# Kernel optimization log

Hardware: AMD Instinct MI355X
Metric: run time of the kernel (lower is better)

The kernel has to match this reference:

```python
import jax, jax.numpy as jnp
import numpy as np

N, E, IN, ED, H = 50000, 500000, 27, 12, 128
LAYERS = 3


def _bn(h, g, b):
    # BatchNorm1d, training-mode batch statistics, biased variance, eps=1e-5
    mu = h.mean(0)
    var = h.var(0)
    return (h - mu) * jax.lax.rsqrt(var + 1e-5) * g + b


def _layer(x, src, dst, ea, eps, eW, eb, W1, b1, g1, be1, W2, b2, ng, nb):
    # GINEConv: project edge_attr to node dim, message = relu(x_j + e), sum-aggregate
    e = ea @ eW + eb                                   # [E, in_dim]
    m = jax.nn.relu(x[src] + e)                        # [E, in_dim]
    agg = jax.ops.segment_sum(m, dst, num_segments=N)  # [N, in_dim]
    h = (1.0 + eps) * x + agg
    # conv MLP: Linear -> BN -> ReLU -> (Dropout eval=id) -> Linear
    h = jax.nn.relu(_bn(h @ W1 + b1, g1, be1))
    h = h @ W2 + b2
    # outer BatchNorm -> ReLU -> (Dropout eval=id)
    return jax.nn.relu(_bn(h, ng, nb))


def setup_inputs() -> dict:
    key = jax.random.key(0)
    ks = iter(jax.random.split(key, 64))
    d = {}
    d["x"] = jax.random.normal(next(ks), (N, IN), jnp.float32)
    d["edge_index"] = jax.random.randint(next(ks), (2, E), 0, N, jnp.int32)
    d["edge_attr"] = jax.random.normal(next(ks), (E, ED), jnp.float32)
    for i in range(LAYERS):
        ind = IN if i == 0 else H
        d[f"l{i}_eps"] = jnp.zeros((), jnp.float32)
        d[f"l{i}_eW"] = jax.random.normal(next(ks), (ED, ind), jnp.float32) * 0.1
        d[f"l{i}_eb"] = jnp.zeros((ind,), jnp.float32)
        d[f"l{i}_W1"] = jax.random.normal(next(ks), (ind, 2 * H), jnp.float32) * (1.0 / np.sqrt(ind))
        d[f"l{i}_b1"] = jnp.zeros((2 * H,), jnp.float32)
        d[f"l{i}_g1"] = jnp.ones((2 * H,), jnp.float32)
        d[f"l{i}_be1"] = jnp.zeros((2 * H,), jnp.float32)
        d[f"l{i}_W2"] = jax.random.normal(next(ks), (2 * H, H), jnp.float32) * (1.0 / np.sqrt(2 * H))
        d[f"l{i}_b2"] = jnp.zeros((H,), jnp.float32)
        d[f"l{i}_ng"] = jnp.ones((H,), jnp.float32)
        d[f"l{i}_nb"] = jnp.zeros((H,), jnp.float32)
    return d


def reference(x, edge_index, edge_attr,
              l0_eps, l0_eW, l0_eb, l0_W1, l0_b1, l0_g1, l0_be1, l0_W2, l0_b2, l0_ng, l0_nb,
              l1_eps, l1_eW, l1_eb, l1_W1, l1_b1, l1_g1, l1_be1, l1_W2, l1_b2, l1_ng, l1_nb,
              l2_eps, l2_eW, l2_eb, l2_W1, l2_b1, l2_g1, l2_be1, l2_W2, l2_b2, l2_ng, l2_nb):
    src, dst = edge_index[0], edge_index[1]
    P = [
        (l0_eps, l0_eW, l0_eb, l0_W1, l0_b1, l0_g1, l0_be1, l0_W2, l0_b2, l0_ng, l0_nb),
        (l1_eps, l1_eW, l1_eb, l1_W1, l1_b1, l1_g1, l1_be1, l1_W2, l1_b2, l1_ng, l1_nb),
        (l2_eps, l2_eW, l2_eb, l2_W1, l2_b1, l2_g1, l2_be1, l2_W2, l2_b2, l2_ng, l2_nb),
    ]
    h = x
    for i, p in enumerate(P):
        out = _layer(h, src, dst, edge_attr, *p)
        if 0 < i < LAYERS - 1 and out.shape == h.shape:
            h = h + 0.3 * out
        else:
            h = out
    return h
```

## Files before the change

### kernel.cpp

```cpp
#include <hip/hip_runtime.h>
#include <hip/hip_bf16.h>


typedef __attribute__((ext_vector_type(8))) short bf16x8;
typedef __attribute__((ext_vector_type(4))) float f32x4;

static inline int cdiv(int a, int b) { return (a + b - 1) / b; }

__device__ inline ushort f2bf(float f) {
    uint32_t u = __float_as_uint(f);
    return (ushort)((u + 0x7FFFu + ((u >> 16) & 1u)) >> 16);
}
__device__ inline float bf2f(ushort h) { return __uint_as_float(((uint32_t)h) << 16); }

__global__ __launch_bounds__(256) void histogram_dst(const int* __restrict__ dst,
                                                     int* __restrict__ deg, int E) {
    int i = blockIdx.x * blockDim.x + threadIdx.x;
    int stride = gridDim.x * blockDim.x;
    for (; i < E; i += stride) atomicAdd(&deg[dst[i]], 1);
}

__global__ __launch_bounds__(1024) void scan_deg(const int* __restrict__ deg,
                                                 int* __restrict__ rowptr, int N) {
    __shared__ int part[1024];
    int t = threadIdx.x;
    int chunk = (N + 1023) / 1024;
    int b = t * chunk;
    int e = b + chunk;
    if (b > N) b = N;
    if (e > N) e = N;
    int s = 0;
    for (int i = b; i < e; ++i) s += deg[i];
    part[t] = s;
    __syncthreads();
    for (int off = 1; off < 1024; off <<= 1) {
        int v = (t >= off) ? part[t - off] : 0;
        __syncthreads();
        part[t] += v;
        __syncthreads();
    }
    int base = (t == 0) ? 0 : part[t - 1];
    for (int i = b; i < e; ++i) {
        rowptr[i] = base;
        base += deg[i];
    }
    if (t == 1023) rowptr[N] = base;
}

__global__ __launch_bounds__(256) void scatter_edges(const int* __restrict__ dst,
                                                     int* __restrict__ cursor,
                                                     int* __restrict__ eid, int E) {
    int i = blockIdx.x * blockDim.x + threadIdx.x;
    int stride = gridDim.x * blockDim.x;
    for (; i < E; i += stride) {
        int pos = atomicAdd(&cursor[dst[i]], 1);
        eid[pos] = i;
    }
}

template <int IND>
__global__ __launch_bounds__(256) void gather_kernel(
    const int* __restrict__ rowptr, const int* __restrict__ eid, const int* __restrict__ src,
    const float* __restrict__ ea, const float* __restrict__ eW, const float* __restrict__ eb,
    const float* __restrict__ x, const float* __restrict__ epsp, float* __restrict__ agg, int N) {
    __shared__ __align__(16) float sW[12 * IND];
    __shared__ __align__(16) float sb[IND];
    int tid = threadIdx.x;
    for (int i = tid; i < 12 * IND; i += 256) sW[i] = eW[i];
    for (int i = tid; i < IND; i += 256) sb[i] = eb[i];
    __syncthreads();

    float onePlusEps = 1.0f + *epsp;
    int lane = tid & 31;
    int n = blockIdx.x * 8 + (tid >> 5);
    if (n >= N) return;
    int beg = rowptr[n], end = rowptr[n + 1];

    if constexpr (IND == 128) {
        int d0 = lane << 2;
        float4 acc = make_float4(0.f, 0.f, 0.f, 0.f);
        float4 bb = *(const float4*)&sb[d0];
        int i = beg;
        for (; i + 2 <= end; i += 2) {
            int e0 = eid[i], e1 = eid[i + 1];
            int s0 = src[e0], s1 = src[e1];
            float av0 = (lane < 12) ? ea[(size_t)e0 * 12 + lane] : 0.0f;
            float av1 = (lane < 12) ? ea[(size_t)e1 * 12 + lane] : 0.0f;
            float4 x0 = *(const float4*)&x[(size_t)s0 * 128 + d0];
            float4 x1 = *(const float4*)&x[(size_t)s1 * 128 + d0];
            float4 p0 = bb, p1 = bb;
#pragma unroll
            for (int k = 0; k < 12; ++k) {
                float a0 = __shfl(av0, k, 32);
                float a1 = __shfl(av1, k, 32);
                float4 w = *(const float4*)&sW[k * 128 + d0];
                p0.x = fmaf(a0, w.x, p0.x); p0.y = fmaf(a0, w.y, p0.y);
                p0.z = fmaf(a0, w.z, p0.z); p0.w = fmaf(a0, w.w, p0.w);
                p1.x = fmaf(a1, w.x, p1.x); p1.y = fmaf(a1, w.y, p1.y);
                p1.z = fmaf(a1, w.z, p1.z); p1.w = fmaf(a1, w.w, p1.w);
            }
            acc.x += fmaxf(x0.x + p0.x, 0.f) + fmaxf(x1.x + p1.x, 0.f);
            acc.y += fmaxf(x0.y + p0.y, 0.f) + fmaxf(x1.y + p1.y, 0.f);
            acc.z += fmaxf(x0.z + p0.z, 0.f) + fmaxf(x1.z + p1.z, 0.f);
            acc.w += fmaxf(x0.w + p0.w, 0.f) + fmaxf(x1.w + p1.w, 0.f);
        }
        if (i < end) {
            int e = eid[i];
            int s = src[e];
            float av = (lane < 12) ? ea[(size_t)e * 12 + lane] : 0.0f;
            float4 p = bb;
#pragma unroll
            for (int k = 0; k < 12; ++k) {
                float ak = __shfl(av, k, 32);
                float4 w = *(const float4*)&sW[k * 128 + d0];
                p.x = fmaf(ak, w.x, p.x); p.y = fmaf(ak, w.y, p.y);
                p.z = fmaf(ak, w.z, p.z); p.w = fmaf(ak, w.w, p.w);
            }
            float4 xv = *(const float4*)&x[(size_t)s * 128 + d0];
            acc.x += fmaxf(xv.x + p.x, 0.f);
            acc.y += fmaxf(xv.y + p.y, 0.f);
            acc.z += fmaxf(xv.z + p.z, 0.f);
            acc.w += fmaxf(xv.w + p.w, 0.f);
        }
        float4 xn = *(const float4*)&x[(size_t)n * 128 + d0];
        float4 o;
        o.x = fmaf(onePlusEps, xn.x, acc.x);
        o.y = fmaf(onePlusEps, xn.y, acc.y);
        o.z = fmaf(onePlusEps, xn.z, acc.z);
        o.w = fmaf(onePlusEps, xn.w, acc.w);
        *(float4*)&agg[(size_t)n * 128 + d0] = o;
    } else {
        int d = lane;
        float acc = 0.0f;
        float bb = (d < IND) ? sb[d] : 0.0f;
        for (int i = beg; i < end; ++i) {
            int e = eid[i];
            int s = src[e];
            float av = (lane < 12) ? ea[(size_t)e * 12 + lane] : 0.0f;
            float p = bb;
#pragma unroll
            for (int k = 0; k < 12; ++k) {
                float ak = __shfl(av, k, 32);
                if (d < IND) p = fmaf(ak, sW[k * IND + d], p);
            }
            if (d < IND) acc += fmaxf(x[(size_t)s * IND + d] + p, 0.0f);
        }
        if (d < IND) agg[(size_t)n * IND + d] = fmaf(onePlusEps, x[(size_t)n * IND + d], acc);
    }
}

__global__ __launch_bounds__(256) void repack_w(const float* __restrict__ W, int K, int N,
                                                ushort* __restrict__ hi, ushort* __restrict__ lo) {
    int kg = (K + 31) / 32;
    int total = (N / 16) * kg * 64;
    int idx = blockIdx.x * 256 + threadIdx.x;
    if (idx >= total) return;
    int l = idx & 63;
    int g = (idx >> 6) % kg;
    int t = (idx >> 6) / kg;
#pragma unroll
    for (int j = 0; j < 8; ++j) {
        int k = g * 32 + ((l >> 4) << 3) + j;
        int n = (t << 4) + (l & 15);
        float v = (k < K) ? W[(size_t)k * N + n] : 0.0f;
        ushort h = f2bf(v);
        hi[(size_t)idx * 8 + j] = h;
        lo[(size_t)idx * 8 + j] = f2bf(v - bf2f(h));
    }
}

template <bool PRE_BN>
__global__ __launch_bounds__(256) void mfma_gemm(const float* __restrict__ A, int M, int K,
                                                 const ushort* __restrict__ Wph,
                                                 const ushort* __restrict__ Wpl,
                                                 const float* __restrict__ bias,
                                                 const float* __restrict__ scale,
                                                 const float* __restrict__ shift,
                                                 float* __restrict__ C, int ldc,
                                                 float* __restrict__ sums,
                                                 float* __restrict__ sumsq) {
    __shared__ __align__(16) ushort As_hi[128 * 32];
    __shared__ __align__(16) ushort As_lo[128 * 32];
    int tid = threadIdx.x;
    int lane = tid & 63;
    int wv = tid >> 6;
    int wm = wv >> 1, wn = wv & 1;
    int row0 = blockIdx.x * 128;
    int col0 = blockIdx.y * 64;
    int kg = (K + 31) >> 5;

    f32x4 acc[4][2] = {};

    for (int g = 0; g < kg; ++g) {
        int k0 = g << 5;
        for (int c = tid; c < 1024; c += 256) {
            int row = c >> 3;
            int kc = (c & 7) << 2;
            int gm = row0 + row;
            float v[4] = {0.f, 0.f, 0.f, 0.f};
            if (gm < M) {
                const float* ap = &A[(size_t)gm * K + k0 + kc];
                if (k0 + kc + 4 <= K) {
                    float4 t4 = *(const float4*)ap;
                    v[0] = t4.x; v[1] = t4.y; v[2] = t4.z; v[3] = t4.w;
                } else {
#pragma unroll
                    for (int t = 0; t < 4; ++t)
                        if (k0 + kc + t < K) v[t] = ap[t];
                }
                if (PRE_BN) {
#pragma unroll
                    for (int t = 0; t < 4; ++t) {
                        int k = k0 + kc + t;
                        if (k < K) v[t] = fmaxf(fmaf(v[t], scale[k], shift[k]), 0.0f);
                    }
                }
            }
            ushort h[4], l2[4];
#pragma unroll
            for (int t = 0; t < 4; ++t) {
                h[t] = f2bf(v[t]);
                l2[t] = f2bf(v[t] - bf2f(h[t]));
            }
            int e = row * 32 + kc;
            *(ushort4*)&As_hi[e] = make_ushort4(h[0], h[1], h[2], h[3]);
            *(ushort4*)&As_lo[e] = make_ushort4(l2[0], l2[1], l2[2], l2[3]);
        }
        __syncthreads();

        bf16x8 bh[2], bl[2], ah[4], al[4];
#pragma unroll
        for (int nf = 0; nf < 2; ++nf) {
            int tn = (col0 >> 4) + (wn << 1) + nf;
            size_t off = (((size_t)tn * kg + g) * 64 + lane) * 8;
            bh[nf] = *(const bf16x8*)(Wph + off);
            bl[nf] = *(const bf16x8*)(Wpl + off);
        }
#pragma unroll
        for (int mf = 0; mf < 4; ++mf) {
            int e = ((wm << 6) + (mf << 4) + (lane & 15)) * 32 + ((lane >> 4) << 3);
            ah[mf] = *(const bf16x8*)&As_hi[e];
            al[mf] = *(const bf16x8*)&As_lo[e];
        }
#pragma unroll
        for (int mf = 0; mf < 4; ++mf)
#pragma unroll
            for (int nf = 0; nf < 2; ++nf) {
                acc[mf][nf] =
                    __builtin_amdgcn_mfma_f32_16x16x32_bf16(ah[mf], bh[nf], acc[mf][nf], 0, 0, 0);
                acc[mf][nf] =
                    __builtin_amdgcn_mfma_f32_16x16x32_bf16(ah[mf], bl[nf], acc[mf][nf], 0, 0, 0);
                acc[mf][nf] =
                    __builtin_amdgcn_mfma_f32_16x16x32_bf16(al[mf], bh[nf], acc[mf][nf], 0, 0, 0);
            }
        __syncthreads();
    }

#pragma unroll
    for (int nf = 0; nf < 2; ++nf) {
        int col = col0 + (wn << 5) + (nf << 4) + (lane & 15);
        float bv = bias[col];
        float s = 0.f, qs = 0.f;
#pragma unroll
        for (int mf = 0; mf < 4; ++mf) {
            int rbase = row0 + (wm << 6) + (mf << 4) + ((lane >> 4) << 2);
#pragma unroll
            for (int q = 0; q < 4; ++q) {
                int row = rbase + q;
                if (row < M) {
                    float v = acc[mf][nf][q] + bv;
                    C[(size_t)row * ldc + col] = v;
                    s += v;
                    qs = fmaf(v, v, qs);
                }
            }
        }
        s += __shfl_xor(s, 16);
        s += __shfl_xor(s, 32);
        qs += __shfl_xor(qs, 16);
        qs += __shfl_xor(qs, 32);
        if (lane < 16) {
            atomicAdd(&sums[col], s);
            atomicAdd(&sumsq[col], qs);
        }
    }
}

__global__ void finalize_bn(const float* __restrict__ sums, const float* __restrict__ sumsq,
                            const float* __restrict__ g, const float* __restrict__ b,
                            float* __restrict__ scale, float* __restrict__ shift, int C,
                            float invN) {
    int c = blockIdx.x * blockDim.x + threadIdx.x;
    if (c < C) {
        float mu = sums[c] * invN;
        float var = sumsq[c] * invN - mu * mu;
        float inv = rsqrtf(var + 1e-5f);
        float sc = g[c] * inv;
        scale[c] = sc;
        shift[c] = b[c] - mu * sc;
    }
}

template <bool RES>
__global__ __launch_bounds__(256) void bn_apply(const float* __restrict__ h,
                                                const float* __restrict__ scale,
                                                const float* __restrict__ shift,
                                                const float* __restrict__ xprev,
                                                float* __restrict__ out, int total4) {
    int i = blockIdx.x * blockDim.x + threadIdx.x;
    int stride = gridDim.x * blockDim.x;
    for (; i < total4; i += stride) {
        int c0 = (i & 31) << 2;
        float4 v = ((const float4*)h)[i];
        float4 o;
        o.x = fmaxf(fmaf(v.x, scale[c0 + 0], shift[c0 + 0]), 0.0f);
        o.y = fmaxf(fmaf(v.y, scale[c0 + 1], shift[c0 + 1]), 0.0f);
        o.z = fmaxf(fmaf(v.z, scale[c0 + 2], shift[c0 + 2]), 0.0f);
        o.w = fmaxf(fmaf(v.w, scale[c0 + 3], shift[c0 + 3]), 0.0f);
        if (RES) {
            float4 xp = ((const float4*)xprev)[i];
            o.x = fmaf(0.3f, o.x, xp.x);
            o.y = fmaf(0.3f, o.y, xp.y);
            o.z = fmaf(0.3f, o.z, xp.z);
            o.w = fmaf(0.3f, o.w, xp.w);
        }
        ((float4*)out)[i] = o;
    }
}

extern "C" void kernel_launch(void* const* d_in, const int* in_sizes, int n_in, void* d_out,
                              int out_size, void* d_ws, size_t ws_size, hipStream_t stream) {
    const float* x_in = (const float*)d_in[0];
    const int* ei = (const int*)d_in[1];
    const float* ea = (const float*)d_in[2];
    const int IN_DIM = 27;
    const int H = 128;
    int N = in_sizes[0] / IN_DIM;
    int E = in_sizes[1] / 2;
    const int* src = ei;
    const int* dst = ei + E;

    auto L = [&](int layer, int j) -> const float* {
        return (const float*)d_in[3 + 11 * layer + j];
    };

    float* X0 = (float*)d_ws;
    float* AGG = X0 + (size_t)N * H;
    float* H1 = AGG + (size_t)N * H;
    float* STATS = H1 + (size_t)N * 2 * H;
    float* sums1 = STATS;
    float* sq1 = STATS + 256;
    float* sums2 = STATS + 512;
    float* sq2 = STATS + 640;
    float* scale1 = STATS + 768;
    float* shift1 = STATS + 1024;
    float* scale2 = STATS + 1280;
    float* shift2 = STATS + 1408;
    int* rowptr = (int*)(STATS + 1536);
    int* cursor = rowptr + (N + 1);
    int* eid = cursor + N;
    size_t wp_off = ((size_t)(eid + E - (int*)d_ws) * 4 + 15) & ~(size_t)15;
    ushort* Wp1h = (ushort*)((char*)d_ws + wp_off);
    ushort* Wp1l = Wp1h + 32768;
    ushort* Wp2h = Wp1l + 32768;
    ushort* Wp2l = Wp2h + 32768;
    float* X1 = (float*)d_out;

    float invN = 1.0f / (float)N;
    int gridM = cdiv(N, 128);
    int gatherG = cdiv(N, 8);

    hipMemsetAsync(rowptr, 0, (size_t)(N + 1) * sizeof(int), stream);
    histogram_dst<<<1024, 256, 0, stream>>>(dst, rowptr, E);
    scan_deg<<<1, 1024, 0, stream>>>(rowptr, cursor, N);
    hipMemcpyAsync(rowptr, cursor, (size_t)(N + 1) * sizeof(int), hipMemcpyDeviceToDevice, stream);
    scatter_edges<<<1024, 256, 0, stream>>>(dst, cursor, eid, E);

    for (int i = 0; i < 3; ++i) {
        int ind = (i == 0) ? IN_DIM : H;
        const float* xin = (i == 0) ? x_in : ((i == 1) ? X0 : X1);
        float* xout = (i == 2) ? (float*)d_out : ((i == 0) ? X0 : X1);

        hipMemsetAsync(STATS, 0, 768 * sizeof(float), stream);

        int kg1 = cdiv(ind, 32);
        int tot1 = 16 * kg1 * 64;
        repack_w<<<cdiv(tot1, 256), 256, 0, stream>>>(L(i, 3), ind, 256, Wp1h, Wp1l);
        int tot2 = 8 * 8 * 64;
        repack_w<<<cdiv(tot2, 256), 256, 0, stream>>>(L(i, 7), 256, 128, Wp2h, Wp2l);

        if (i == 0)
            gather_kernel<27><<<gatherG, 256, 0, stream>>>(rowptr, eid, src, ea, L(i, 1), L(i, 2),
                                                           xin, L(i, 0), AGG, N);
        else
            gather_kernel<128><<<gatherG, 256, 0, stream>>>(rowptr, eid, src, ea, L(i, 1), L(i, 2),
                                                            xin, L(i, 0), AGG, N);

        mfma_gemm<false><<<dim3(gridM, 4), 256, 0, stream>>>(AGG, N, ind, Wp1h, Wp1l, L(i, 4),
                                                             nullptr, nullptr, H1, 256, sums1, sq1);
        finalize_bn<<<1, 256, 0, stream>>>(sums1, sq1, L(i, 5), L(i, 6), scale1, shift1, 256, invN);

        mfma_gemm<true><<<dim3(gridM, 2), 256, 0, stream>>>(H1, N, 256, Wp2h, Wp2l, L(i, 8),
                                                            scale1, shift1, AGG, 128, sums2, sq2);
        finalize_bn<<<1, 256, 0, stream>>>(sums2, sq2, L(i, 9), L(i, 10), scale2, shift2, 128,
                                           invN);

        int total4 = N * H / 4;
        if (i == 1)
            bn_apply<true><<<2048, 256, 0, stream>>>(AGG, scale2, shift2, X0, xout, total4);
        else
            bn_apply<false><<<2048, 256, 0, stream>>>(AGG, scale2, shift2, nullptr, xout, total4);
    }
}
```

Measured before the change: 967.6 us.

## Widen GEMM tiles to full N per block, unroll gather by 4, vectorize layer-0 gather

The MFMA GEMM now uses 512-thread blocks that each cover the full output width, so every A row tile is loaded and split into bf16 hi/lo only once instead of once per column block. The 128-wide gather processes four edges per iteration to keep more independent loads in flight. The 27-wide layer-0 gather splits each 32-lane group into four 8-lane subgroups that each handle a different edge with float4 vectors, then reduces the subgroups with shuffles. In exchange, GEMM blocks carry more accumulators and registers, and the layer-0 path has more complex boundary handling.

```diff
diff --git a/kernel.cpp b/kernel.cpp
--- a/kernel.cpp
+++ b/kernel.cpp
@@ -58,16 +58,15 @@
     }
 }
 
-template <int IND>
-__global__ __launch_bounds__(256) void gather_kernel(
+__global__ __launch_bounds__(256) void gather128(
     const int* __restrict__ rowptr, const int* __restrict__ eid, const int* __restrict__ src,
     const float* __restrict__ ea, const float* __restrict__ eW, const float* __restrict__ eb,
     const float* __restrict__ x, const float* __restrict__ epsp, float* __restrict__ agg, int N) {
-    __shared__ __align__(16) float sW[12 * IND];
-    __shared__ __align__(16) float sb[IND];
+    __shared__ __align__(16) float sW[12 * 128];
+    __shared__ __align__(16) float sb[128];
     int tid = threadIdx.x;
-    for (int i = tid; i < 12 * IND; i += 256) sW[i] = eW[i];
-    for (int i = tid; i < IND; i += 256) sb[i] = eb[i];
+    for (int i = tid; i < 12 * 128; i += 256) sW[i] = eW[i];
+    if (tid < 128) sb[tid] = eb[tid];
     __syncthreads();
 
     float onePlusEps = 1.0f + *epsp;
@@ -75,77 +74,171 @@
     int n = blockIdx.x * 8 + (tid >> 5);
     if (n >= N) return;
     int beg = rowptr[n], end = rowptr[n + 1];
-
-    if constexpr (IND == 128) {
-        int d0 = lane << 2;
-        float4 acc = make_float4(0.f, 0.f, 0.f, 0.f);
-        float4 bb = *(const float4*)&sb[d0];
-        int i = beg;
-        for (; i + 2 <= end; i += 2) {
-            int e0 = eid[i], e1 = eid[i + 1];
-            int s0 = src[e0], s1 = src[e1];
-            float av0 = (lane < 12) ? ea[(size_t)e0 * 12 + lane] : 0.0f;
-            float av1 = (lane < 12) ? ea[(size_t)e1 * 12 + lane] : 0.0f;
-            float4 x0 = *(const float4*)&x[(size_t)s0 * 128 + d0];
-            float4 x1 = *(const float4*)&x[(size_t)s1 * 128 + d0];
-            float4 p0 = bb, p1 = bb;
-#pragma unroll
-            for (int k = 0; k < 12; ++k) {
-                float a0 = __shfl(av0, k, 32);
-                float a1 = __shfl(av1, k, 32);
-                float4 w = *(const float4*)&sW[k * 128 + d0];
-                p0.x = fmaf(a0, w.x, p0.x); p0.y = fmaf(a0, w.y, p0.y);
-                p0.z = fmaf(a0, w.z, p0.z); p0.w = fmaf(a0, w.w, p0.w);
-                p1.x = fmaf(a1, w.x, p1.x); p1.y = fmaf(a1, w.y, p1.y);
-                p1.z = fmaf(a1, w.z, p1.z); p1.w = fmaf(a1, w.w, p1.w);
+    int d0 = lane << 2;
+    float4 bb = *(const float4*)&sb[d0];
+    float4 acc = make_float4(0.f, 0.f, 0.f, 0.f);
+
+    int i = beg;
+    for (; i + 4 <= end; i += 4) {
+        int e[4], s[4];
+        float av[4];
+        float4 xv[4], p[4];
+#pragma unroll
+        for (int j = 0; j < 4; ++j) e[j] = eid[i + j];
+#pragma unroll
+        for (int j = 0; j < 4; ++j) {
+            s[j] = src[e[j]];
+            av[j] = (lane < 12) ? ea[(size_t)e[j] * 12 + lane] : 0.0f;
+        }
+#pragma unroll
+        for (int j = 0; j < 4; ++j) {
+            xv[j] = *(const float4*)&x[(size_t)s[j] * 128 + d0];
+            p[j] = bb;
+        }
+#pragma unroll
+        for (int k = 0; k < 12; ++k) {
+            float4 w = *(const float4*)&sW[k * 128 + d0];
+#pragma unroll
+            for (int j = 0; j < 4; ++j) {
+                float a = __shfl(av[j], k, 32);
+                p[j].x = fmaf(a, w.x, p[j].x);
+                p[j].y = fmaf(a, w.y, p[j].y);
+                p[j].z = fmaf(a, w.z, p[j].z);
+                p[j].w = fmaf(a, w.w, p[j].w);
             }
-            acc.x += fmaxf(x0.x + p0.x, 0.f) + fmaxf(x1.x + p1.x, 0.f);
-            acc.y += fmaxf(x0.y + p0.y, 0.f) + fmaxf(x1.y + p1.y, 0.f);
-            acc.z += fmaxf(x0.z + p0.z, 0.f) + fmaxf(x1.z + p1.z, 0.f);
-            acc.w += fmaxf(x0.w + p0.w, 0.f) + fmaxf(x1.w + p1.w, 0.f);
-        }
-        if (i < end) {
-            int e = eid[i];
-            int s = src[e];
-            float av = (lane < 12) ? ea[(size_t)e * 12 + lane] : 0.0f;
-            float4 p = bb;
-#pragma unroll
-            for (int k = 0; k < 12; ++k) {
-                float ak = __shfl(av, k, 32);
-                float4 w = *(const float4*)&sW[k * 128 + d0];
-                p.x = fmaf(ak, w.x, p.x); p.y = fmaf(ak, w.y, p.y);
-                p.z = fmaf(ak, w.z, p.z); p.w = fmaf(ak, w.w, p.w);
+        }
+#pragma unroll
+        for (int j = 0; j < 4; ++j) {
+            acc.x += fmaxf(xv[j].x + p[j].x, 0.f);
+            acc.y += fmaxf(xv[j].y + p[j].y, 0.f);
+            acc.z += fmaxf(xv[j].z + p[j].z, 0.f);
+            acc.w += fmaxf(xv[j].w + p[j].w, 0.f);
+        }
+    }
+    for (; i < end; ++i) {
+        int e = eid[i];
+        int s = src[e];
+        float av = (lane < 12) ? ea[(size_t)e * 12 + lane] : 0.0f;
+        float4 p = bb;
+#pragma unroll
+        for (int k = 0; k < 12; ++k) {
+            float ak = __shfl(av, k, 32);
+            float4 w = *(const float4*)&sW[k * 128 + d0];
+            p.x = fmaf(ak, w.x, p.x);
+            p.y = fmaf(ak, w.y, p.y);
+            p.z = fmaf(ak, w.z, p.z);
+            p.w = fmaf(ak, w.w, p.w);
+        }
+        float4 xv = *(const float4*)&x[(size_t)s * 128 + d0];
+        acc.x += fmaxf(xv.x + p.x, 0.f);
+        acc.y += fmaxf(xv.y + p.y, 0.f);
+        acc.z += fmaxf(xv.z + p.z, 0.f);
+        acc.w += fmaxf(xv.w + p.w, 0.f);
+    }
+    float4 xn = *(const float4*)&x[(size_t)n * 128 + d0];
+    float4 o;
+    o.x = fmaf(onePlusEps, xn.x, acc.x);
+    o.y = fmaf(onePlusEps, xn.y, acc.y);
+    o.z = fmaf(onePlusEps, xn.z, acc.z);
+    o.w = fmaf(onePlusEps, xn.w, acc.w);
+    *(float4*)&agg[(size_t)n * 128 + d0] = o;
+}
+
+__global__ __launch_bounds__(256) void gather27(
+    const int* __restrict__ rowptr, const int* __restrict__ eid, const int* __restrict__ src,
+    const float* __restrict__ ea, const float* __restrict__ eW, const float* __restrict__ eb,
+    const float* __restrict__ x, const float* __restrict__ epsp, float* __restrict__ agg, int N) {
+    __shared__ __align__(16) float sW[12 * 28 + 4];
+    __shared__ __align__(16) float sb[32];
+    int tid = threadIdx.x;
+    for (int i = tid; i < 12 * 28 + 4; i += 256) sW[i] = 0.0f;
+    if (tid < 32) sb[tid] = 0.0f;
+    __syncthreads();
+    for (int i = tid; i < 12 * 27; i += 256) {
+        int k = i / 27, d = i - k * 27;
+        sW[k * 28 + d] = eW[i];
+    }
+    if (tid < 27) sb[tid] = eb[tid];
+    __syncthreads();
+
+    float onePlusEps = 1.0f + *epsp;
+    int lane = tid & 31;
+    int n = blockIdx.x * 8 + (tid >> 5);
+    if (n >= N) return;
+    int beg = rowptr[n], end = rowptr[n + 1];
+    int sub = lane >> 3, sl = lane & 7;
+    int d0 = sl << 2;
+    int d0c = (sl < 7) ? d0 : 24;
+    float4 bb = *(const float4*)&sb[d0c];
+    float4 acc = make_float4(0.f, 0.f, 0.f, 0.f);
+
+    int iters = (end - beg + 3) >> 2;
+    for (int it = 0; it < iters; ++it) {
+        int i = beg + it * 4 + sub;
+        bool v = i < end;
+        int e = v ? eid[i] : 0;
+        int s = v ? src[e] : 0;
+        float avA = v ? ea[(size_t)e * 12 + sl] : 0.0f;
+        float avB = (v && sl < 4) ? ea[(size_t)e * 12 + 8 + sl] : 0.0f;
+        float4 xv = make_float4(0.f, 0.f, 0.f, 0.f);
+        if (v) {
+            if (sl < 6) {
+                xv = *(const float4*)&x[(size_t)s * 27 + d0];
+            } else if (sl == 6) {
+                xv.x = x[(size_t)s * 27 + 24];
+                xv.y = x[(size_t)s * 27 + 25];
+                xv.z = x[(size_t)s * 27 + 26];
             }
-            float4 xv = *(const float4*)&x[(size_t)s * 128 + d0];
+        }
+        float4 p = bb;
+#pragma unroll
+        for (int k = 0; k < 8; ++k) {
+            float ak = __shfl(avA, k, 8);
+            float4 w = *(const float4*)&sW[k * 28 + d0c];
+            p.x = fmaf(ak, w.x, p.x);
+            p.y = fmaf(ak, w.y, p.y);
+            p.z = fmaf(ak, w.z, p.z);
+            p.w = fmaf(ak, w.w, p.w);
+        }
+#pragma unroll
+        for (int k = 8; k < 12; ++k) {
+            float ak = __shfl(avB, k - 8, 8);
+            float4 w = *(const float4*)&sW[k * 28 + d0c];
+            p.x = fmaf(ak, w.x, p.x);
+            p.y = fmaf(ak, w.y, p.y);
+            p.z = fmaf(ak, w.z, p.z);
+            p.w = fmaf(ak, w.w, p.w);
+        }
+        if (v) {
             acc.x += fmaxf(xv.x + p.x, 0.f);
             acc.y += fmaxf(xv.y + p.y, 0.f);
             acc.z += fmaxf(xv.z + p.z, 0.f);
             acc.w += fmaxf(xv.w + p.w, 0.f);
         }
-        float4 xn = *(const float4*)&x[(size_t)n * 128 + d0];
-        float4 o;
-        o.x = fmaf(onePlusEps, xn.x, acc.x);
-        o.y = fmaf(onePlusEps, xn.y, acc.y);
-        o.z = fmaf(onePlusEps, xn.z, acc.z);
-        o.w = fmaf(onePlusEps, xn.w, acc.w);
-        *(float4*)&agg[(size_t)n * 128 + d0] = o;
-    } else {
-        int d = lane;
-        float acc = 0.0f;
-        float bb = (d < IND) ? sb[d] : 0.0f;
-        for (int i = beg; i < end; ++i) {
-            int e = eid[i];
-            int s = src[e];
-            float av = (lane < 12) ? ea[(size_t)e * 12 + lane] : 0.0f;
-            float p = bb;
-#pragma unroll
-            for (int k = 0; k < 12; ++k) {
-                float ak = __shfl(av, k, 32);
-                if (d < IND) p = fmaf(ak, sW[k * IND + d], p);
-            }
-            if (d < IND) acc += fmaxf(x[(size_t)s * IND + d] + p, 0.0f);
-        }
-        if (d < IND) agg[(size_t)n * IND + d] = fmaf(onePlusEps, x[(size_t)n * IND + d], acc);
+    }
+    acc.x += __shfl_xor(acc.x, 8, 32);
+    acc.y += __shfl_xor(acc.y, 8, 32);
+    acc.z += __shfl_xor(acc.z, 8, 32);
+    acc.w += __shfl_xor(acc.w, 8, 32);
+    acc.x += __shfl_xor(acc.x, 16, 32);
+    acc.y += __shfl_xor(acc.y, 16, 32);
+    acc.z += __shfl_xor(acc.z, 16, 32);
+    acc.w += __shfl_xor(acc.w, 16, 32);
+
+    if (sub == 0) {
+        if (sl < 6) {
+            float4 xn = *(const float4*)&x[(size_t)n * 27 + d0];
+            float4 o;
+            o.x = fmaf(onePlusEps, xn.x, acc.x);
+            o.y = fmaf(onePlusEps, xn.y, acc.y);
+            o.z = fmaf(onePlusEps, xn.z, acc.z);
+            o.w = fmaf(onePlusEps, xn.w, acc.w);
+            *(float4*)&agg[(size_t)n * 27 + d0] = o;
+        } else if (sl == 6) {
+            agg[(size_t)n * 27 + 24] = fmaf(onePlusEps, x[(size_t)n * 27 + 24], acc.x);
+            agg[(size_t)n * 27 + 25] = fmaf(onePlusEps, x[(size_t)n * 27 + 25], acc.y);
+            agg[(size_t)n * 27 + 26] = fmaf(onePlusEps, x[(size_t)n * 27 + 26], acc.z);
+        }
     }
 }
 
@@ -169,8 +262,8 @@
     }
 }
 
-template <bool PRE_BN>
-__global__ __launch_bounds__(256) void mfma_gemm(const float* __restrict__ A, int M, int K,
+template <int NF, bool PRE_BN>
+__global__ __launch_bounds__(512) void mfma_gemm(const float* __restrict__ A, int M, int K,
                                                  const ushort* __restrict__ Wph,
                                                  const ushort* __restrict__ Wpl,
                                                  const float* __restrict__ bias,
@@ -184,16 +277,15 @@
     int tid = threadIdx.x;
     int lane = tid & 63;
     int wv = tid >> 6;
-    int wm = wv >> 1, wn = wv & 1;
+    int wm = wv >> 2, wn = wv & 3;
     int row0 = blockIdx.x * 128;
-    int col0 = blockIdx.y * 64;
     int kg = (K + 31) >> 5;
 
-    f32x4 acc[4][2] = {};
+    f32x4 acc[4][NF] = {};
 
     for (int g = 0; g < kg; ++g) {
         int k0 = g << 5;
-        for (int c = tid; c < 1024; c += 256) {
+        for (int c = tid; c < 1024; c += 512) {
             int row = c >> 3;
             int kc = (c & 7) << 2;
             int gm = row0 + row;
@@ -228,14 +320,7 @@
         }
         __syncthreads();
 
-        bf16x8 bh[2], bl[2], ah[4], al[4];
-#pragma unroll
-        for (int nf = 0; nf < 2; ++nf) {
-            int tn = (col0 >> 4) + (wn << 1) + nf;
-            size_t off = (((size_t)tn * kg + g) * 64 + lane) * 8;
-            bh[nf] = *(const bf16x8*)(Wph + off);
-            bl[nf] = *(const bf16x8*)(Wpl + off);
-        }
+        bf16x8 ah[4], al[4];
 #pragma unroll
         for (int mf = 0; mf < 4; ++mf) {
             int e = ((wm << 6) + (mf << 4) + (lane & 15)) * 32 + ((lane >> 4) << 3);
@@ -243,22 +328,27 @@
             al[mf] = *(const bf16x8*)&As_lo[e];
         }
 #pragma unroll
-        for (int mf = 0; mf < 4; ++mf)
-#pragma unroll
-            for (int nf = 0; nf < 2; ++nf) {
+        for (int nf = 0; nf < NF; ++nf) {
+            int tn = wn * NF + nf;
+            size_t off = (((size_t)tn * kg + g) * 64 + lane) * 8;
+            bf16x8 bh = *(const bf16x8*)(Wph + off);
+            bf16x8 bl = *(const bf16x8*)(Wpl + off);
+#pragma unroll
+            for (int mf = 0; mf < 4; ++mf) {
                 acc[mf][nf] =
-                    __builtin_amdgcn_mfma_f32_16x16x32_bf16(ah[mf], bh[nf], acc[mf][nf], 0, 0, 0);
+                    __builtin_amdgcn_mfma_f32_16x16x32_bf16(ah[mf], bh, acc[mf][nf], 0, 0, 0);
                 acc[mf][nf] =
-                    __builtin_amdgcn_mfma_f32_16x16x32_bf16(ah[mf], bl[nf], acc[mf][nf], 0, 0, 0);
+                    __builtin_amdgcn_mfma_f32_16x16x32_bf16(ah[mf], bl, acc[mf][nf], 0, 0, 0);
                 acc[mf][nf] =
-                    __builtin_amdgcn_mfma_f32_16x16x32_bf16(al[mf], bh[nf], acc[mf][nf], 0, 0, 0);
+                    __builtin_amdgcn_mfma_f32_16x16x32_bf16(al[mf], bh, acc[mf][nf], 0, 0, 0);
             }
+        }
         __syncthreads();
     }
 
 #pragma unroll
-    for (int nf = 0; nf < 2; ++nf) {
-        int col = col0 + (wn << 5) + (nf << 4) + (lane & 15);
+    for (int nf = 0; nf < NF; ++nf) {
+        int col = (wn * NF + nf) * 16 + (lane & 15);
         float bv = bias[col];
         float s = 0.f, qs = 0.f;
 #pragma unroll
@@ -390,18 +480,18 @@
         repack_w<<<cdiv(tot2, 256), 256, 0, stream>>>(L(i, 7), 256, 128, Wp2h, Wp2l);
 
         if (i == 0)
-            gather_kernel<27><<<gatherG, 256, 0, stream>>>(rowptr, eid, src, ea, L(i, 1), L(i, 2),
-                                                           xin, L(i, 0), AGG, N);
+            gather27<<<gatherG, 256, 0, stream>>>(rowptr, eid, src, ea, L(i, 1), L(i, 2), xin,
+                                                  L(i, 0), AGG, N);
         else
-            gather_kernel<128><<<gatherG, 256, 0, stream>>>(rowptr, eid, src, ea, L(i, 1), L(i, 2),
-                                                            xin, L(i, 0), AGG, N);
-
-        mfma_gemm<false><<<dim3(gridM, 4), 256, 0, stream>>>(AGG, N, ind, Wp1h, Wp1l, L(i, 4),
-                                                             nullptr, nullptr, H1, 256, sums1, sq1);
+            gather128<<<gatherG, 256, 0, stream>>>(rowptr, eid, src, ea, L(i, 1), L(i, 2), xin,
+                                                   L(i, 0), AGG, N);
+
+        mfma_gemm<4, false><<<gridM, 512, 0, stream>>>(AGG, N, ind, Wp1h, Wp1l, L(i, 4), nullptr,
+                                                       nullptr, H1, 256, sums1, sq1);
         finalize_bn<<<1, 256, 0, stream>>>(sums1, sq1, L(i, 5), L(i, 6), scale1, shift1, 256, invN);
 
-        mfma_gemm<true><<<dim3(gridM, 2), 256, 0, stream>>>(H1, N, 256, Wp2h, Wp2l, L(i, 8),
-                                                            scale1, shift1, AGG, 128, sums2, sq2);
+        mfma_gemm<2, true><<<gridM, 512, 0, stream>>>(H1, N, 256, Wp2h, Wp2l, L(i, 8), scale1,
+                                                      shift1, AGG, 128, sums2, sq2);
         finalize_bn<<<1, 256, 0, stream>>>(sums2, sq2, L(i, 9), L(i, 10), scale2, shift2, 128,
                                            invN);
 
```

Result: faster. 821.1 us (-15.1%).
